# Kernel tuning notes

Measured on AMD Instinct MI355X. Metric: run time of the kernel, lower is better.

## Reference

```python
import jax, jax.numpy as jnp
import numpy as np

N = 100000          # number of agents
H = 1024            # hidden_dim
GS = 8              # grid_size
NB = 4.0            # neighborhood radius (L-inf)


def setup_inputs() -> dict:
    key = jax.random.key(0)
    k1, k2, k3, k4 = jax.random.split(key, 4)
    h_states = jax.random.normal(k1, (N, H), dtype=jnp.float32)
    positions = jax.random.uniform(k2, (N, 2), dtype=jnp.float32) * 20.0 - 10.0  # in [-10,10]
    W = jax.random.normal(k3, (H, H), dtype=jnp.float32) * (1.0 / np.sqrt(H))  # embed.weight
    b = jax.random.normal(k4, (H,), dtype=jnp.float32) * 0.01                  # embed.bias
    return {"h_states": h_states, "positions": positions, "idx": 5, "W": W, "b": b}


def reference(h_states, positions, idx, W, b):
    n = h_states.shape[0]
    diff = positions - positions[idx]                      # (N,2) relative positions
    mask = (jnp.max(jnp.abs(diff), axis=1) <= NB) & (jnp.arange(n) != idx)
    # torch does float clamp to [0, GS-1] then int() truncation (== floor since >=0)
    val = jnp.clip((diff / NB + 1.0) * 0.5 * GS, 0.0, GS - 1)
    g = jnp.floor(val).astype(jnp.int32)                   # (N,2) -> (gx, gy)
    cell = g[:, 1] * GS + g[:, 0]                          # (N,)
    mf = mask.astype(h_states.dtype)
    grid = jax.ops.segment_sum(h_states * mf[:, None], cell, num_segments=GS * GS)  # (GS*GS, H)
    counts = jax.ops.segment_sum(mf, cell, num_segments=GS * GS)                    # (GS*GS,)
    counts = jnp.maximum(counts, 1.0)
    pooled = (grid / counts[:, None]).sum(axis=0)          # (H,)
    return pooled @ W.T + b
```

## Files before the change

### kernel.cpp

```cpp
#include <hip/hip_runtime.h>

#define HDIM 1024
#define GS 8
#define NBR 4.0f
#define CELLS_APB 2048
#define NSP 32

__launch_bounds__(256)
__global__ void k_cells(const float2* __restrict__ pos, const int* __restrict__ idxp,
                        int n, unsigned char* __restrict__ cellv,
                        int* __restrict__ hist_g, float* __restrict__ partials)
{
    __shared__ int hist[64];
    int tid = threadIdx.x;
    if (tid < 64) hist[tid] = 0;
    __syncthreads();

    int idx = idxp[0];
    float2 p0 = pos[idx];

    int a0 = blockIdx.x * CELLS_APB + tid * 8;

    if (a0 + 8 <= n) {
        const float4* pp = (const float4*)pos;
        unsigned long long packed = 0;
#pragma unroll
        for (int k = 0; k < 4; ++k) {
            float4 q = pp[(a0 >> 1) + k];
#pragma unroll
            for (int half = 0; half < 2; ++half) {
                int i = a0 + k * 2 + half;
                float dx = (half ? q.z : q.x) - p0.x;
                float dy = (half ? q.w : q.y) - p0.y;
                bool msk = (fmaxf(fabsf(dx), fabsf(dy)) <= NBR) && (i != idx);
                unsigned long long cv = 0xFF;
                if (msk) {
                    float vx = fminf(fmaxf((dx / NBR + 1.0f) * 0.5f * (float)GS, 0.0f), (float)(GS - 1));
                    float vy = fminf(fmaxf((dy / NBR + 1.0f) * 0.5f * (float)GS, 0.0f), (float)(GS - 1));
                    int c = (int)vy * GS + (int)vx;
                    cv = (unsigned long long)c;
                    atomicAdd(&hist[c], 1);
                }
                packed |= cv << ((k * 2 + half) * 8);
            }
        }
        *(unsigned long long*)(cellv + a0) = packed;
    } else {
        for (int k = 0; k < 8; ++k) {
            int i = a0 + k;
            if (i < n) {
                float2 p = pos[i];
                float dx = p.x - p0.x, dy = p.y - p0.y;
                bool msk = (fmaxf(fabsf(dx), fabsf(dy)) <= NBR) && (i != idx);
                unsigned char cv = 0xFF;
                if (msk) {
                    float vx = fminf(fmaxf((dx / NBR + 1.0f) * 0.5f * (float)GS, 0.0f), (float)(GS - 1));
                    float vy = fminf(fmaxf((dy / NBR + 1.0f) * 0.5f * (float)GS, 0.0f), (float)(GS - 1));
                    int c = (int)vy * GS + (int)vx;
                    cv = (unsigned char)c;
                    atomicAdd(&hist[c], 1);
                }
                cellv[i] = cv;
            }
        }
    }
    __syncthreads();
    if (tid < 64) hist_g[blockIdx.x * 64 + tid] = hist[tid];
    if (blockIdx.x < NSP)
        ((float4*)(partials + (size_t)blockIdx.x * HDIM))[tid] = make_float4(0.f, 0.f, 0.f, 0.f);
}

__launch_bounds__(256)
__global__ void k_reduce(const float* __restrict__ h, const unsigned char* __restrict__ cellv,
                         const int* __restrict__ hist_g, int nbc, int n,
                         float* __restrict__ partials)
{
    __shared__ int   cnt[64];
    __shared__ float inv[65];
    __shared__ int   llist[264];
    __shared__ int   wcnt[4];

    int tid  = threadIdx.x;
    int wave = tid >> 6, lane = tid & 63;

    if (tid < 64) cnt[tid] = 0;
    __syncthreads();

    {
        int s = 0;
        int b = wave;
        for (; b + 16 <= nbc; b += 16) {
            int x0 = hist_g[(b     ) * 64 + lane];
            int x1 = hist_g[(b +  4) * 64 + lane];
            int x2 = hist_g[(b +  8) * 64 + lane];
            int x3 = hist_g[(b + 12) * 64 + lane];
            s += x0 + x1 + x2 + x3;
        }
        for (; b < nbc; b += 4) s += hist_g[b * 64 + lane];
        atomicAdd(&cnt[lane], s);
    }
    __syncthreads();
    if (tid < 64) inv[tid] = 1.0f / (float)(cnt[tid] > 1 ? cnt[tid] : 1);
    if (tid == 64) inv[64] = 0.0f;

    int i = blockIdx.x * 256 + tid;
    unsigned char cv = (i < n) ? cellv[i] : (unsigned char)0xFF;
    bool m = (cv != 0xFF);
    unsigned long long bal = __ballot(m);
    if (lane == 0) wcnt[wave] = __popcll(bal);
    int ppos = __popcll(bal & ((1ull << lane) - 1ull));
    __syncthreads();

    int off = 0;
    for (int w2 = 0; w2 < wave; ++w2) off += wcnt[w2];
    int lc = wcnt[0] + wcnt[1] + wcnt[2] + wcnt[3];
    int lcp = (lc + 7) & ~7;
    if (m) llist[off + ppos] = (i << 8) | (int)cv;
    if (tid >= lc && tid < lcp) llist[tid] = 64;
    __syncthreads();

    if (lcp == 0) return;

    float4 acc = make_float4(0.f, 0.f, 0.f, 0.f);
    for (int g = 0; g < lcp; g += 8) {
        int e[8];
        float4 v[8];
#pragma unroll
        for (int k = 0; k < 8; ++k) e[k] = llist[g + k];
#pragma unroll
        for (int k = 0; k < 8; ++k)
            v[k] = ((const float4*)(h + (size_t)(e[k] >> 8) * HDIM))[tid];
#pragma unroll
        for (int k = 0; k < 8; ++k) {
            float w = inv[e[k] & 255];
            acc.x += w * v[k].x; acc.y += w * v[k].y;
            acc.z += w * v[k].z; acc.w += w * v[k].w;
        }
    }

    float* pr = partials + (size_t)(blockIdx.x & (NSP - 1)) * HDIM + tid * 4;
    atomicAdd(&pr[0], acc.x);
    atomicAdd(&pr[1], acc.y);
    atomicAdd(&pr[2], acc.z);
    atomicAdd(&pr[3], acc.w);
}

__launch_bounds__(256)
__global__ void k_matvec(const float* __restrict__ W, const float* __restrict__ bvec,
                         const float* __restrict__ partials, float* __restrict__ out)
{
    __shared__ float pooled_s[HDIM];
    int tid  = threadIdx.x;
    int wave = tid >> 6, lane = tid & 63;

    float4 s = make_float4(0.f, 0.f, 0.f, 0.f);
#pragma unroll 8
    for (int r = 0; r < NSP; ++r) {
        float4 v = ((const float4*)(partials + (size_t)r * HDIM))[tid];
        s.x += v.x; s.y += v.y; s.z += v.z; s.w += v.w;
    }
    ((float4*)pooled_s)[tid] = s;
    __syncthreads();

    int j = blockIdx.x * 4 + wave;
    const float4* Wr = (const float4*)(W + (size_t)j * HDIM);
    float d = 0.f;
#pragma unroll
    for (int q = 0; q < 4; ++q) {
        float4 wv = Wr[lane + q * 64];
        float4 pv = ((const float4*)pooled_s)[lane + q * 64];
        d += wv.x * pv.x + wv.y * pv.y + wv.z * pv.z + wv.w * pv.w;
    }

    for (int offr = 32; offr > 0; offr >>= 1)
        d += __shfl_down(d, offr, 64);

    if (lane == 0)
        out[j] = d + bvec[j];
}

extern "C" void kernel_launch(void* const* d_in, const int* in_sizes, int n_in,
                              void* d_out, int out_size, void* d_ws, size_t ws_size,
                              hipStream_t stream) {
    const float*  h    = (const float*)d_in[0];
    const float2* pos  = (const float2*)d_in[1];
    const int*    idxp = (const int*)d_in[2];
    const float*  W    = (const float*)d_in[3];
    const float*  bvec = (const float*)d_in[4];
    float* out = (float*)d_out;

    int n = in_sizes[0] / HDIM;

    int nbc = (n + CELLS_APB - 1) / CELLS_APB;
    int nbr = (n + 255) / 256;

    char* ws = (char*)d_ws;
    unsigned char* cellv = (unsigned char*)ws;
    size_t off1 = (((size_t)n) + 255) & ~(size_t)255;
    int*   hist_g = (int*)(ws + off1);
    size_t off2 = (off1 + (size_t)nbc * 64 * 4 + 255) & ~(size_t)255;
    float* partials = (float*)(ws + off2);

    k_cells <<<nbc, 256, 0, stream>>>(pos, idxp, n, cellv, hist_g, partials);
    k_reduce<<<nbr, 256, 0, stream>>>(h, cellv, hist_g, nbc, n, partials);
    k_matvec<<<HDIM / 4, 256, 0, stream>>>(W, bvec, partials, out);
}
```

Before: 30.36 us.

## Recompute agent cells in reduce kernel instead of storing per-agent cell bytes

The first kernel now only builds per-block cell histograms and no longer writes a per-agent cell byte array. The reduce kernel recomputes each agent's mask and cell from positions, overlapping this with the histogram summation. The first kernel also covers 4096 agents per block instead of 2048, which halves the histogram rows the reduce kernel must sum. In exchange, positions are read twice (8 bytes per agent rather than 1) and the cell arithmetic is done twice.

```diff
diff --git a/kernel.cpp b/kernel.cpp
--- a/kernel.cpp
+++ b/kernel.cpp
@@ -3,13 +3,22 @@
 #define HDIM 1024
 #define GS 8
 #define NBR 4.0f
-#define CELLS_APB 2048
+#define HIST_APB 4096
 #define NSP 32
 
+__device__ __forceinline__ int agent_cell(float px, float py, float p0x, float p0y,
+                                          int i, int idx, bool* m)
+{
+    float dx = px - p0x, dy = py - p0y;
+    *m = (fmaxf(fabsf(dx), fabsf(dy)) <= NBR) && (i != idx);
+    float vx = fminf(fmaxf((dx / NBR + 1.0f) * 0.5f * (float)GS, 0.0f), (float)(GS - 1));
+    float vy = fminf(fmaxf((dy / NBR + 1.0f) * 0.5f * (float)GS, 0.0f), (float)(GS - 1));
+    return (int)vy * GS + (int)vx;
+}
+
 __launch_bounds__(256)
-__global__ void k_cells(const float2* __restrict__ pos, const int* __restrict__ idxp,
-                        int n, unsigned char* __restrict__ cellv,
-                        int* __restrict__ hist_g, float* __restrict__ partials)
+__global__ void k_hist(const float2* __restrict__ pos, const int* __restrict__ idxp,
+                       int n, int* __restrict__ hist_g, float* __restrict__ partials)
 {
     __shared__ int hist[64];
     int tid = threadIdx.x;
@@ -19,61 +28,41 @@
     int idx = idxp[0];
     float2 p0 = pos[idx];
 
-    int a0 = blockIdx.x * CELLS_APB + tid * 8;
+    int a0 = blockIdx.x * HIST_APB + tid * 16;
 
-    if (a0 + 8 <= n) {
+    if (a0 + 16 <= n) {
         const float4* pp = (const float4*)pos;
-        unsigned long long packed = 0;
 #pragma unroll
-        for (int k = 0; k < 4; ++k) {
+        for (int k = 0; k < 8; ++k) {
             float4 q = pp[(a0 >> 1) + k];
-#pragma unroll
-            for (int half = 0; half < 2; ++half) {
-                int i = a0 + k * 2 + half;
-                float dx = (half ? q.z : q.x) - p0.x;
-                float dy = (half ? q.w : q.y) - p0.y;
-                bool msk = (fmaxf(fabsf(dx), fabsf(dy)) <= NBR) && (i != idx);
-                unsigned long long cv = 0xFF;
-                if (msk) {
-                    float vx = fminf(fmaxf((dx / NBR + 1.0f) * 0.5f * (float)GS, 0.0f), (float)(GS - 1));
-                    float vy = fminf(fmaxf((dy / NBR + 1.0f) * 0.5f * (float)GS, 0.0f), (float)(GS - 1));
-                    int c = (int)vy * GS + (int)vx;
-                    cv = (unsigned long long)c;
-                    atomicAdd(&hist[c], 1);
-                }
-                packed |= cv << ((k * 2 + half) * 8);
-            }
+            bool m0, m1;
+            int c0 = agent_cell(q.x, q.y, p0.x, p0.y, a0 + k * 2,     idx, &m0);
+            int c1 = agent_cell(q.z, q.w, p0.x, p0.y, a0 + k * 2 + 1, idx, &m1);
+            if (m0) atomicAdd(&hist[c0], 1);
+            if (m1) atomicAdd(&hist[c1], 1);
         }
-        *(unsigned long long*)(cellv + a0) = packed;
     } else {
-        for (int k = 0; k < 8; ++k) {
+        for (int k = 0; k < 16; ++k) {
             int i = a0 + k;
             if (i < n) {
                 float2 p = pos[i];
-                float dx = p.x - p0.x, dy = p.y - p0.y;
-                bool msk = (fmaxf(fabsf(dx), fabsf(dy)) <= NBR) && (i != idx);
-                unsigned char cv = 0xFF;
-                if (msk) {
-                    float vx = fminf(fmaxf((dx / NBR + 1.0f) * 0.5f * (float)GS, 0.0f), (float)(GS - 1));
-                    float vy = fminf(fmaxf((dy / NBR + 1.0f) * 0.5f * (float)GS, 0.0f), (float)(GS - 1));
-                    int c = (int)vy * GS + (int)vx;
-                    cv = (unsigned char)c;
-                    atomicAdd(&hist[c], 1);
-                }
-                cellv[i] = cv;
+                bool m;
+                int c = agent_cell(p.x, p.y, p0.x, p0.y, i, idx, &m);
+                if (m) atomicAdd(&hist[c], 1);
             }
         }
     }
     __syncthreads();
     if (tid < 64) hist_g[blockIdx.x * 64 + tid] = hist[tid];
-    if (blockIdx.x < NSP)
-        ((float4*)(partials + (size_t)blockIdx.x * HDIM))[tid] = make_float4(0.f, 0.f, 0.f, 0.f);
+
+    for (int r = blockIdx.x; r < NSP; r += gridDim.x)
+        ((float4*)(partials + (size_t)r * HDIM))[tid] = make_float4(0.f, 0.f, 0.f, 0.f);
 }
 
 __launch_bounds__(256)
-__global__ void k_reduce(const float* __restrict__ h, const unsigned char* __restrict__ cellv,
-                         const int* __restrict__ hist_g, int nbc, int n,
-                         float* __restrict__ partials)
+__global__ void k_reduce(const float* __restrict__ h, const float2* __restrict__ pos,
+                         const int* __restrict__ idxp, const int* __restrict__ hist_g,
+                         int nbh, int n, float* __restrict__ partials)
 {
     __shared__ int   cnt[64];
     __shared__ float inv[65];
@@ -88,24 +77,25 @@
 
     {
         int s = 0;
-        int b = wave;
-        for (; b + 16 <= nbc; b += 16) {
-            int x0 = hist_g[(b     ) * 64 + lane];
-            int x1 = hist_g[(b +  4) * 64 + lane];
-            int x2 = hist_g[(b +  8) * 64 + lane];
-            int x3 = hist_g[(b + 12) * 64 + lane];
-            s += x0 + x1 + x2 + x3;
-        }
-        for (; b < nbc; b += 4) s += hist_g[b * 64 + lane];
+        for (int b = wave; b < nbh; b += 4)
+            s += hist_g[b * 64 + lane];
         atomicAdd(&cnt[lane], s);
     }
+
+    int idx = idxp[0];
+    float2 p0 = pos[idx];
+    int i = blockIdx.x * 256 + tid;
+    bool m = false;
+    int cv = 0;
+    if (i < n) {
+        float2 p = pos[i];
+        cv = agent_cell(p.x, p.y, p0.x, p0.y, i, idx, &m);
+    }
+
     __syncthreads();
     if (tid < 64) inv[tid] = 1.0f / (float)(cnt[tid] > 1 ? cnt[tid] : 1);
     if (tid == 64) inv[64] = 0.0f;
 
-    int i = blockIdx.x * 256 + tid;
-    unsigned char cv = (i < n) ? cellv[i] : (unsigned char)0xFF;
-    bool m = (cv != 0xFF);
     unsigned long long bal = __ballot(m);
     if (lane == 0) wcnt[wave] = __popcll(bal);
     int ppos = __popcll(bal & ((1ull << lane) - 1ull));
@@ -115,7 +105,7 @@
     for (int w2 = 0; w2 < wave; ++w2) off += wcnt[w2];
     int lc = wcnt[0] + wcnt[1] + wcnt[2] + wcnt[3];
     int lcp = (lc + 7) & ~7;
-    if (m) llist[off + ppos] = (i << 8) | (int)cv;
+    if (m) llist[off + ppos] = (i << 8) | cv;
     if (tid >= lc && tid < lcp) llist[tid] = 64;
     __syncthreads();
 
@@ -191,17 +181,15 @@
 
     int n = in_sizes[0] / HDIM;
 
-    int nbc = (n + CELLS_APB - 1) / CELLS_APB;
+    int nbh = (n + HIST_APB - 1) / HIST_APB;
     int nbr = (n + 255) / 256;
 
     char* ws = (char*)d_ws;
-    unsigned char* cellv = (unsigned char*)ws;
-    size_t off1 = (((size_t)n) + 255) & ~(size_t)255;
-    int*   hist_g = (int*)(ws + off1);
-    size_t off2 = (off1 + (size_t)nbc * 64 * 4 + 255) & ~(size_t)255;
-    float* partials = (float*)(ws + off2);
+    int*   hist_g   = (int*)ws;
+    size_t off1     = ((size_t)nbh * 64 * 4 + 255) & ~(size_t)255;
+    float* partials = (float*)(ws + off1);
 
-    k_cells <<<nbc, 256, 0, stream>>>(pos, idxp, n, cellv, hist_g, partials);
-    k_reduce<<<nbr, 256, 0, stream>>>(h, cellv, hist_g, nbc, n, partials);
+    k_hist  <<<nbh, 256, 0, stream>>>(pos, idxp, n, hist_g, partials);
+    k_reduce<<<nbr, 256, 0, stream>>>(h, pos, idxp, hist_g, nbh, n, partials);
     k_matvec<<<HDIM / 4, 256, 0, stream>>>(W, bvec, partials, out);
 }
```

Result: no change. 30.36 us (+0.0%).
